# Kernel optimization log

Hardware: AMD Instinct MI355X
Metric: run time of the kernel (lower is better)

The kernel has to match this reference:

```python
import jax, jax.numpy as jnp
import numpy as np

N_NODES, N_EDGES = 100000, 800000
F_NODE, F_EDGE, N_CLASSES = 128, 16, 10


def _lin(key, fan_in, fan_out, bias=True):
    k1, k2 = jax.random.split(key)
    W = jax.random.normal(k1, (fan_in, fan_out), jnp.float32) * 0.05
    if bias:
        b = jax.random.normal(k2, (fan_out,), jnp.float32) * 0.05
        return W, b
    return (W,)


def setup_inputs() -> dict:
    key = jax.random.key(0)
    ks = jax.random.split(key, 24)
    inp = {
        "x": jax.random.normal(ks[0], (N_NODES, F_NODE), jnp.float32),
        "edge_index": jax.random.randint(ks[1], (2, N_EDGES), 0, N_NODES, jnp.int64 if jax.config.jax_enable_x64 else jnp.int32),
        "edge_attr": jax.random.normal(ks[2], (N_EDGES, F_EDGE), jnp.float32),
    }
    dims = [(F_NODE, 128), (128, 128), (128, 256)]  # (in_channels, out_channels) per layer
    i = 3
    for li, (din, dout) in enumerate(dims, start=1):
        inp[f"Wq{li}"], inp[f"bq{li}"] = _lin(ks[i], din, dout); i += 1
        inp[f"Wk{li}"], inp[f"bk{li}"] = _lin(ks[i], din, dout); i += 1
        inp[f"Wv{li}"], inp[f"bv{li}"] = _lin(ks[i], din, dout); i += 1
        (inp[f"We{li}"],) = _lin(ks[i], F_EDGE, dout, bias=False); i += 1  # PyG lin_edge: bias=False
        inp[f"Ws{li}"], inp[f"bs{li}"] = _lin(ks[i], din, dout); i += 1  # root/skip weight
    inp["Wc"], inp["bc"] = _lin(ks[i], 256, N_CLASSES)
    return inp


def transformer_conv(x, src, dst, edge_attr, Wq, bq, Wk, bk, Wv, bv, We, Ws, bs):
    """PyG TransformerConv, heads=1, concat=True, root_weight=True."""
    N = x.shape[0]
    C = Wq.shape[1]
    q = x @ Wq + bq                      # [N, C]
    k = x @ Wk + bk                      # [N, C]
    v = x @ Wv + bv                      # [N, C]
    e = edge_attr @ We                   # [E, C] edge-conditioned term
    # per-edge attention logits: <q_i, k_j + e_ij> / sqrt(C)
    alpha = jnp.sum(q[dst] * (k[src] + e), axis=-1) / jnp.sqrt(jnp.float32(C))  # [E]
    # segment softmax over edges sharing a destination node
    m = jax.ops.segment_max(alpha, dst, num_segments=N)
    p = jnp.exp(alpha - m[dst])
    s = jax.ops.segment_sum(p, dst, num_segments=N)
    a = p / (s[dst] + 1e-16)
    # scatter-aggregate weighted messages (value_j + edge term)
    out = jax.ops.segment_sum(a[:, None] * (v[src] + e), dst, num_segments=N)  # [N, C]
    return out + x @ Ws + bs             # root/skip connection


def reference(x, edge_index, edge_attr,
              Wq1, bq1, Wk1, bk1, Wv1, bv1, We1, Ws1, bs1,
              Wq2, bq2, Wk2, bk2, Wv2, bv2, We2, Ws2, bs2,
              Wq3, bq3, Wk3, bk3, Wv3, bv3, We3, Ws3, bs3,
              Wc, bc):
    src, dst = edge_index[0], edge_index[1]
    h = transformer_conv(x, src, dst, edge_attr, Wq1, bq1, Wk1, bk1, Wv1, bv1, We1, Ws1, bs1)
    h = jax.nn.relu(h)  # dropout is identity in eval mode
    h = transformer_conv(h, src, dst, edge_attr, Wq2, bq2, Wk2, bk2, Wv2, bv2, We2, Ws2, bs2)
    h = jax.nn.relu(h)
    h = transformer_conv(h, src, dst, edge_attr, Wq3, bq3, Wk3, bk3, Wv3, bv3, We3, Ws3, bs3)
    return h @ Wc + bc                   # [N, num_classes]
```

## Files before the change

### kernel.cpp

```cpp
#include <hip/hip_runtime.h>
#include <math.h>


typedef unsigned int uint;
typedef unsigned short ushort;
typedef __bf16 bf16x8 __attribute__((ext_vector_type(8)));
typedef float f32x4 __attribute__((ext_vector_type(4)));

__device__ __forceinline__ ushort f2bf(float f) {
    uint u = __float_as_uint(f);
    u += 0x7fffu + ((u >> 16) & 1u);
    return (ushort)(u >> 16);
}
__device__ __forceinline__ float bf2f(ushort h) {
    return __uint_as_float(((uint)h) << 16);
}
__device__ __forceinline__ void unpack8(uint4 t, float* o) {
    o[0] = bf2f((ushort)(t.x & 0xffffu)); o[1] = bf2f((ushort)(t.x >> 16));
    o[2] = bf2f((ushort)(t.y & 0xffffu)); o[3] = bf2f((ushort)(t.y >> 16));
    o[4] = bf2f((ushort)(t.z & 0xffffu)); o[5] = bf2f((ushort)(t.z >> 16));
    o[6] = bf2f((ushort)(t.w & 0xffffu)); o[7] = bf2f((ushort)(t.w >> 16));
}

__global__ void k_zero(uint* p, int n) {
    int i = blockIdx.x * 256 + threadIdx.x;
    if (i < n) p[i] = 0u;
}

__global__ void k_hist(const int* __restrict__ dst, uint* __restrict__ counts, int E, int N) {
    int e = blockIdx.x * 256 + threadIdx.x;
    if (e < E) {
        int d = dst[e];
        d = (d < 0) ? 0 : (d >= N ? N - 1 : d);
        atomicAdd(&counts[d], 1u);
    }
}

__global__ void k_scan1(const uint* __restrict__ counts, uint* __restrict__ bsum, int n) {
    __shared__ uint sm[256];
    int tid = threadIdx.x;
    int base = blockIdx.x * 1024 + tid * 4;
    uint s = 0;
#pragma unroll
    for (int j = 0; j < 4; ++j)
        if (base + j < n) s += counts[base + j];
    sm[tid] = s;
    __syncthreads();
    for (int d = 128; d > 0; d >>= 1) {
        if (tid < d) sm[tid] += sm[tid + d];
        __syncthreads();
    }
    if (tid == 0) bsum[blockIdx.x] = sm[0];
}

__global__ void k_scan2(uint* bsum, int nb) {
    if (threadIdx.x == 0 && blockIdx.x == 0) {
        uint run = 0;
        for (int i = 0; i < nb; ++i) { uint v = bsum[i]; bsum[i] = run; run += v; }
    }
}

__global__ void k_scan3(const uint* __restrict__ counts, const uint* __restrict__ bsum,
                        uint* __restrict__ row_ptr, int n, int E) {
    __shared__ uint sm[256];
    int tid = threadIdx.x;
    int base = blockIdx.x * 1024 + tid * 4;
    uint local[4];
    uint s = 0;
#pragma unroll
    for (int j = 0; j < 4; ++j) {
        local[j] = (base + j < n) ? counts[base + j] : 0u;
        s += local[j];
    }
    sm[tid] = s;
    __syncthreads();
    for (int d = 1; d < 256; d <<= 1) {
        uint v = (tid >= d) ? sm[tid - d] : 0u;
        __syncthreads();
        sm[tid] += v;
        __syncthreads();
    }
    uint run = sm[tid] - s + bsum[blockIdx.x];
#pragma unroll
    for (int j = 0; j < 4; ++j)
        if (base + j < n) { row_ptr[base + j] = run; run += local[j]; }
    if (blockIdx.x == 0 && tid == 0) row_ptr[n] = (uint)E;
}

__global__ void k_fill(const int* __restrict__ ei, const uint* __restrict__ row_ptr,
                       uint* __restrict__ cursor, int2* __restrict__ srcid, int E, int N) {
    int e = blockIdx.x * 256 + threadIdx.x;
    if (e >= E) return;
    int s = ei[e];
    int d = ei[E + e];
    s = (s < 0) ? 0 : (s >= N ? N - 1 : s);
    d = (d < 0) ? 0 : (d >= N ? N - 1 : d);
    uint idx = row_ptr[d] + atomicAdd(&cursor[d], 1u);
    srcid[idx] = make_int2(s, e);
}

__global__ void k_cvt(const float4* __restrict__ in, ushort4* __restrict__ outp, int n4) {
    int i = blockIdx.x * 256 + threadIdx.x;
    if (i >= n4) return;
    float4 v = in[i];
    ushort4 o;
    o.x = f2bf(v.x); o.y = f2bf(v.y); o.z = f2bf(v.z); o.w = f2bf(v.w);
    outp[i] = o;
}

__global__ void k_packg(const float* __restrict__ Wq, const float* __restrict__ bq,
                        const float* __restrict__ We, float* __restrict__ Wgf,
                        float* __restrict__ bgf, int C) {
    int id = blockIdx.x * 256 + threadIdx.x;
    if (id < 2048) {
        int k = id >> 4, f = id & 15;
        float s = 0.f;
        for (int c = 0; c < C; ++c) s = fmaf(Wq[k * C + c], We[f * C + c], s);
        Wgf[id] = s;
    } else if (id < 2064) {
        int f = id - 2048;
        float s = 0.f;
        for (int c = 0; c < C; ++c) s = fmaf(bq[c], We[f * C + c], s);
        bgf[f] = s;
    }
}

__global__ void k_packw(const float* __restrict__ Wq, const float* __restrict__ Wk,
                        const float* __restrict__ Wv, const float* __restrict__ Ws,
                        const float* __restrict__ Wgf, ushort* __restrict__ Bp, int C) {
    int nct = (4 * C + 16) >> 4;
    int total = 4 * nct * 512;
    int id = blockIdx.x * 256 + threadIdx.x;
    if (id >= total) return;
    int j = id & 7;
    int rest = id >> 3;
    int lane = rest & 63;
    rest >>= 6;
    int ct = rest % nct;
    int kt = rest / nct;
    int k = kt * 32 + ((lane >> 4) << 3) + j;
    int c = (ct << 4) + (lane & 15);
    float w;
    if (c < 4 * C) {
        int mat = c / C, cc = c % C;
        const float* W = (mat == 0) ? Wq : (mat == 1) ? Wk : (mat == 2) ? Wv : Ws;
        w = W[k * C + cc];
    } else {
        w = Wgf[k * 16 + (c - 4 * C)];
    }
    Bp[id] = f2bf(w);
}

__global__ void k_bias(const float* __restrict__ bq, const float* __restrict__ bk,
                       const float* __restrict__ bv, const float* __restrict__ bs,
                       const float* __restrict__ bgf, float* __restrict__ outp, int C) {
    int c = blockIdx.x * 256 + threadIdx.x;
    if (c >= 4 * C + 16) return;
    float v;
    if (c < 4 * C) {
        int mat = c / C, cc = c % C;
        const float* b = (mat == 0) ? bq : (mat == 1) ? bk : (mat == 2) ? bv : bs;
        v = b[cc];
    } else {
        v = bgf[c - 4 * C];
    }
    outp[c] = v;
}

__global__ __launch_bounds__(256) void k_gemm(const ushort* __restrict__ A,
                                              const ushort* __restrict__ Bp,
                                              const float* __restrict__ bias,
                                              ushort* __restrict__ H,
                                              ushort* __restrict__ S,
                                              ushort* __restrict__ g, int C) {
    int fourC = 4 * C, threeC = 3 * C;
    int P = fourC + 16;
    int nct = P >> 4;
    int lane = threadIdx.x & 63;
    int wave = threadIdx.x >> 6;
    int quad = lane >> 4;
    int r = lane & 15;
    int m0 = blockIdx.y << 4;
    int c0 = (blockIdx.x << 8) + (wave << 6);
    int ct0 = c0 >> 4;
    if (ct0 >= nct) return;
    int row = m0 + r;

    f32x4 acc[4];
#pragma unroll
    for (int i = 0; i < 4; ++i) acc[i] = (f32x4){0.f, 0.f, 0.f, 0.f};

#pragma unroll
    for (int kk = 0; kk < 4; ++kk) {
        bf16x8 a = *(const bf16x8*)(A + (size_t)row * 128 + kk * 32 + (quad << 3));
#pragma unroll
        for (int i = 0; i < 4; ++i) {
            if (ct0 + i < nct) {
                bf16x8 b = *(const bf16x8*)(Bp + ((size_t)((kk * nct + ct0 + i) << 6) + lane) * 8);
                acc[i] = __builtin_amdgcn_mfma_f32_16x16x32_bf16(a, b, acc[i], 0, 0, 0);
            }
        }
    }
#pragma unroll
    for (int i = 0; i < 4; ++i) {
        int cc = c0 + (i << 4) + r;
        if (cc >= P) continue;
        float bi = bias[cc];
#pragma unroll
        for (int reg = 0; reg < 4; ++reg) {
            int rr = m0 + (quad << 2) + reg;
            ushort val = f2bf(acc[i][reg] + bi);
            if (cc < threeC)      H[(size_t)rr * threeC + cc] = val;
            else if (cc < fourC)  S[(size_t)rr * C + (cc - threeC)] = val;
            else                  g[(size_t)rr * 16 + (cc - fourC)] = val;
        }
    }
}

template <int C, int GSIZE, bool RELU>
__global__ __launch_bounds__(256, 6) void k_edge(const ushort* __restrict__ H,
                                                 ushort* __restrict__ S,
                                                 const ushort* __restrict__ g,
                                                 const uint* __restrict__ row_ptr,
                                                 const int2* __restrict__ srcid,
                                                 const float* __restrict__ eattr,
                                                 const float* __restrict__ We,
                                                 int N) {
    constexpr int VR = C / GSIZE;
    constexpr int TH = 3 * C;
    constexpr int GPB = 256 / GSIZE;
    __shared__ float swex[GPB][17];
    const float scale = (C == 128) ? 0.08838834764831843f : 0.0625f;
    const float foldk = 16.0f / (float)GSIZE;

    int lane = threadIdx.x & (GSIZE - 1);
    int grp = threadIdx.x / GSIZE;
    int f = lane & 15;
    int node = blockIdx.x * GPB + grp;
    if (node >= N) return;

    float q[VR];
    {
        uint4 tt = *(const uint4*)(H + (size_t)node * TH + lane * VR);
        unpack8(tt, q);
    }
    float gl = bf2f(g[(size_t)node * 16 + f]);
    uint beg = row_ptr[node], end = row_ptr[node + 1];

    float l = 0.f, w = 0.f;
    float acc[VR];
#pragma unroll
    for (int j = 0; j < VR; ++j) acc[j] = 0.f;

    for (uint t = beg; t < end; t += 2) {
        bool has1 = (t + 1 < end);
        int2 se0 = srcid[t];
        int2 se1 = has1 ? srcid[t + 1] : se0;
        float at0 = eattr[(size_t)se0.y * 16 + f];
        float at1 = eattr[(size_t)se1.y * 16 + f];
        uint4 k0 = *(const uint4*)(H + (size_t)se0.x * TH + C + lane * VR);
        uint4 v0 = *(const uint4*)(H + (size_t)se0.x * TH + 2 * C + lane * VR);
        uint4 k1, v1;
        if (has1) {
            k1 = *(const uint4*)(H + (size_t)se1.x * TH + C + lane * VR);
            v1 = *(const uint4*)(H + (size_t)se1.x * TH + 2 * C + lane * VR);
        }
        float kf[VR];
        unpack8(k0, kf);
        float p0 = foldk * at0 * gl;
#pragma unroll
        for (int j = 0; j < VR; ++j) p0 = fmaf(q[j], kf[j], p0);
        float p1 = 0.f;
        if (has1) {
            unpack8(k1, kf);
            p1 = foldk * at1 * gl;
#pragma unroll
            for (int j = 0; j < VR; ++j) p1 = fmaf(q[j], kf[j], p1);
        }
        p0 += __shfl_xor(p0, 1); p1 += __shfl_xor(p1, 1);
        p0 += __shfl_xor(p0, 2); p1 += __shfl_xor(p1, 2);
        p0 += __shfl_xor(p0, 4); p1 += __shfl_xor(p1, 4);
        p0 += __shfl_xor(p0, 8); p1 += __shfl_xor(p1, 8);
        if (GSIZE == 32) { p0 += __shfl_xor(p0, 16); p1 += __shfl_xor(p1, 16); }
        float e0 = __expf(p0 * scale);
        float e1 = has1 ? __expf(p1 * scale) : 0.f;
        l += e0 + e1;
        w = fmaf(e0, at0, w);
        w = fmaf(e1, at1, w);
        float vf[VR];
        unpack8(v0, vf);
#pragma unroll
        for (int j = 0; j < VR; ++j) acc[j] = fmaf(e0, vf[j], acc[j]);
        if (has1) {
            unpack8(v1, vf);
#pragma unroll
            for (int j = 0; j < VR; ++j) acc[j] = fmaf(e1, vf[j], acc[j]);
        }
    }

    float inv = 1.f / (l + 1e-16f);
    if (lane < 16) swex[grp][lane] = w;
    float ew[VR];
#pragma unroll
    for (int j = 0; j < VR; ++j) ew[j] = 0.f;
#pragma unroll
    for (int f2 = 0; f2 < 16; ++f2) {
        float wf = swex[grp][f2];
        const float* wrow = We + f2 * C + lane * VR;
#pragma unroll
        for (int u = 0; u < VR / 4; ++u) {
            float4 cv = *(const float4*)(wrow + u * 4);
            ew[u * 4 + 0] = fmaf(wf, cv.x, ew[u * 4 + 0]);
            ew[u * 4 + 1] = fmaf(wf, cv.y, ew[u * 4 + 1]);
            ew[u * 4 + 2] = fmaf(wf, cv.z, ew[u * 4 + 2]);
            ew[u * 4 + 3] = fmaf(wf, cv.w, ew[u * 4 + 3]);
        }
    }
    ushort* srow = S + (size_t)node * C + lane * VR;
    uint4 skv = *(const uint4*)srow;
    float sk[8];
    unpack8(skv, sk);
    uint4 ov;
    uint* op = (uint*)&ov;
#pragma unroll
    for (int h = 0; h < 4; ++h) {
        float o0 = (acc[2 * h] + ew[2 * h]) * inv + sk[2 * h];
        float o1 = (acc[2 * h + 1] + ew[2 * h + 1]) * inv + sk[2 * h + 1];
        if (RELU) { o0 = fmaxf(o0, 0.f); o1 = fmaxf(o1, 0.f); }
        op[h] = (uint)f2bf(o0) | ((uint)f2bf(o1) << 16);
    }
    *(uint4*)srow = ov;
}

__global__ void k_cls(const ushort* __restrict__ h, const float* __restrict__ Wc,
                      const float* __restrict__ bc, float* __restrict__ outp, int N) {
    int t = blockIdx.x * 256 + threadIdx.x;
    int node = t >> 4;
    int c = t & 15;
    if (node >= N || c >= 10) return;
    const ushort* hr = h + (size_t)node * 256;
    float acc = 0.f;
#pragma unroll 4
    for (int k4 = 0; k4 < 64; ++k4) {
        uint2 u = *(const uint2*)(hr + k4 * 4);
        float h0 = bf2f((ushort)(u.x & 0xffffu));
        float h1 = bf2f((ushort)(u.x >> 16));
        float h2 = bf2f((ushort)(u.y & 0xffffu));
        float h3 = bf2f((ushort)(u.y >> 16));
        int kb = k4 * 4;
        acc = fmaf(h0, Wc[(kb + 0) * 10 + c], acc);
        acc = fmaf(h1, Wc[(kb + 1) * 10 + c], acc);
        acc = fmaf(h2, Wc[(kb + 2) * 10 + c], acc);
        acc = fmaf(h3, Wc[(kb + 3) * 10 + c], acc);
    }
    outp[node * 10 + c] = acc + bc[c];
}

extern "C" void kernel_launch(void* const* d_in, const int* in_sizes, int n_in,
                              void* d_out, int out_size, void* d_ws, size_t ws_size,
                              hipStream_t stream) {
    const float* x = (const float*)d_in[0];
    const int* ei = (const int*)d_in[1];
    const float* eattr = (const float*)d_in[2];
    const int N = in_sizes[0] / 128;
    const int E = in_sizes[1] / 2;

    const float* Wq[3], *bq[3], *Wk[3], *bk[3], *Wv[3], *bv[3], *We[3], *Ws[3], *bs[3];
    for (int li = 0; li < 3; ++li) {
        int base = 3 + li * 9;
        Wq[li] = (const float*)d_in[base + 0];
        bq[li] = (const float*)d_in[base + 1];
        Wk[li] = (const float*)d_in[base + 2];
        bk[li] = (const float*)d_in[base + 3];
        Wv[li] = (const float*)d_in[base + 4];
        bv[li] = (const float*)d_in[base + 5];
        We[li] = (const float*)d_in[base + 6];
        Ws[li] = (const float*)d_in[base + 7];
        bs[li] = (const float*)d_in[base + 8];
    }
    const float* Wc = (const float*)d_in[30];
    const float* bc = (const float*)d_in[31];

    size_t off = 0;
    char* base = (char*)d_ws;
    auto alloc = [&](size_t bytes) -> void* {
        void* p = base + off;
        off = (off + bytes + 255) & ~(size_t)255;
        return p;
    };
    ushort* SA = (ushort*)alloc((size_t)N * 256 * 2);
    ushort* SB = (ushort*)alloc((size_t)N * 128 * 2);
    ushort* H  = (ushort*)alloc((size_t)N * 768 * 2);
    ushort* gbuf = (ushort*)alloc((size_t)N * 16 * 2);
    ushort* Bp = (ushort*)alloc(140000 * 2);
    float* biasc = (float*)alloc(1040 * 4);
    float* Wgf = (float*)alloc(2048 * 4);
    float* bgf = (float*)alloc(16 * 4);
    uint* row_ptr = (uint*)alloc((size_t)(N + 1) * 4);
    uint* counts = (uint*)alloc((size_t)N * 4);
    uint* cursor = (uint*)alloc((size_t)N * 4);
    uint* bsum = (uint*)alloc(1024 * 4);
    int2* srcid = (int2*)alloc((size_t)E * 8);

    ushort* xb = SB;

    int nb = (N + 1023) / 1024;

    k_zero<<<(N + 255) / 256, 256, 0, stream>>>(counts, N);
    k_zero<<<(N + 255) / 256, 256, 0, stream>>>(cursor, N);
    k_hist<<<(E + 255) / 256, 256, 0, stream>>>(ei + E, counts, E, N);
    k_scan1<<<nb, 256, 0, stream>>>(counts, bsum, N);
    k_scan2<<<1, 64, 0, stream>>>(bsum, nb);
    k_scan3<<<nb, 256, 0, stream>>>(counts, bsum, row_ptr, N, E);
    k_fill<<<(E + 255) / 256, 256, 0, stream>>>(ei, row_ptr, cursor, srcid, E, N);

    int n4 = N * 128 / 4;
    k_cvt<<<(n4 + 255) / 256, 256, 0, stream>>>((const float4*)x, (ushort4*)xb, n4);

    for (int li = 0; li < 3; ++li) {
        int C = (li == 2) ? 256 : 128;
        int P = 4 * C + 16;
        int packTotal = 4 * (P >> 4) * 512;
        const ushort* A = (li == 0) ? xb : (li == 1) ? SA : SB;
        ushort* Sout = (li == 1) ? SB : SA;

        k_packg<<<9, 256, 0, stream>>>(Wq[li], bq[li], We[li], Wgf, bgf, C);
        k_packw<<<(packTotal + 255) / 256, 256, 0, stream>>>(Wq[li], Wk[li], Wv[li], Ws[li], Wgf, Bp, C);
        k_bias<<<(P + 255) / 256, 256, 0, stream>>>(bq[li], bk[li], bv[li], bs[li], bgf, biasc, C);
        k_gemm<<<dim3((P + 255) / 256, N / 16), 256, 0, stream>>>(A, Bp, biasc, H, Sout, gbuf, C);
        if (li == 2)
            k_edge<256, 32, false><<<(N * 32 + 255) / 256, 256, 0, stream>>>(H, Sout, gbuf, row_ptr, srcid, eattr, We[li], N);
        else
            k_edge<128, 16, true><<<(N * 16 + 255) / 256, 256, 0, stream>>>(H, Sout, gbuf, row_ptr, srcid, eattr, We[li], N);
    }

    k_cls<<<(N * 16 + 255) / 256, 256, 0, stream>>>(SA, Wc, bc, (float*)d_out, N);
}
```

Baseline: 1.021 ms.

## Register-tile GEMM over 64 rows and fuse small setup kernels

The projection GEMM now has each wave compute four 16-row tiles per B fragment, so every B load from the packed weights is reused across 64 rows instead of 16. Out-of-range rows are clamped on load and skipped on store. Separately, weight packing and bias packing are merged into one kernel, and the two zeroing launches become one by allocating counts and cursor contiguously, which cuts launch count. The larger register tile raises VGPR pressure (sixteen accumulators per wave) and may reduce occupancy.

```diff
diff --git a/kernel.cpp b/kernel.cpp
--- a/kernel.cpp
+++ b/kernel.cpp
@@ -125,46 +125,46 @@
     }
 }
 
-__global__ void k_packw(const float* __restrict__ Wq, const float* __restrict__ Wk,
-                        const float* __restrict__ Wv, const float* __restrict__ Ws,
-                        const float* __restrict__ Wgf, ushort* __restrict__ Bp, int C) {
-    int nct = (4 * C + 16) >> 4;
+__global__ void k_packwb(const float* __restrict__ Wq, const float* __restrict__ bq,
+                         const float* __restrict__ Wk, const float* __restrict__ bk,
+                         const float* __restrict__ Wv, const float* __restrict__ bv,
+                         const float* __restrict__ Ws, const float* __restrict__ bs,
+                         const float* __restrict__ Wgf, const float* __restrict__ bgf,
+                         ushort* __restrict__ Bp, float* __restrict__ biasc, int C) {
+    int P = 4 * C + 16;
+    int nct = P >> 4;
     int total = 4 * nct * 512;
     int id = blockIdx.x * 256 + threadIdx.x;
-    if (id >= total) return;
-    int j = id & 7;
-    int rest = id >> 3;
-    int lane = rest & 63;
-    rest >>= 6;
-    int ct = rest % nct;
-    int kt = rest / nct;
-    int k = kt * 32 + ((lane >> 4) << 3) + j;
-    int c = (ct << 4) + (lane & 15);
-    float w;
-    if (c < 4 * C) {
-        int mat = c / C, cc = c % C;
-        const float* W = (mat == 0) ? Wq : (mat == 1) ? Wk : (mat == 2) ? Wv : Ws;
-        w = W[k * C + cc];
-    } else {
-        w = Wgf[k * 16 + (c - 4 * C)];
-    }
-    Bp[id] = f2bf(w);
-}
-
-__global__ void k_bias(const float* __restrict__ bq, const float* __restrict__ bk,
-                       const float* __restrict__ bv, const float* __restrict__ bs,
-                       const float* __restrict__ bgf, float* __restrict__ outp, int C) {
-    int c = blockIdx.x * 256 + threadIdx.x;
-    if (c >= 4 * C + 16) return;
-    float v;
-    if (c < 4 * C) {
-        int mat = c / C, cc = c % C;
-        const float* b = (mat == 0) ? bq : (mat == 1) ? bk : (mat == 2) ? bv : bs;
-        v = b[cc];
-    } else {
-        v = bgf[c - 4 * C];
-    }
-    outp[c] = v;
+    if (id < total) {
+        int j = id & 7;
+        int rest = id >> 3;
+        int lane = rest & 63;
+        rest >>= 6;
+        int ct = rest % nct;
+        int kt = rest / nct;
+        int k = kt * 32 + ((lane >> 4) << 3) + j;
+        int c = (ct << 4) + (lane & 15);
+        float w;
+        if (c < 4 * C) {
+            int mat = c / C, cc = c % C;
+            const float* W = (mat == 0) ? Wq : (mat == 1) ? Wk : (mat == 2) ? Wv : Ws;
+            w = W[k * C + cc];
+        } else {
+            w = Wgf[k * 16 + (c - 4 * C)];
+        }
+        Bp[id] = f2bf(w);
+    } else if (id < total + P) {
+        int c = id - total;
+        float v;
+        if (c < 4 * C) {
+            int mat = c / C, cc = c % C;
+            const float* b = (mat == 0) ? bq : (mat == 1) ? bk : (mat == 2) ? bv : bs;
+            v = b[cc];
+        } else {
+            v = bgf[c - 4 * C];
+        }
+        biasc[c] = v;
+    }
 }
 
 __global__ __launch_bounds__(256) void k_gemm(const ushort* __restrict__ A,
@@ -172,7 +172,7 @@
                                               const float* __restrict__ bias,
                                               ushort* __restrict__ H,
                                               ushort* __restrict__ S,
-                                              ushort* __restrict__ g, int C) {
+                                              ushort* __restrict__ g, int C, int N) {
     int fourC = 4 * C, threeC = 3 * C;
     int P = fourC + 16;
     int nct = P >> 4;
@@ -180,39 +180,51 @@
     int wave = threadIdx.x >> 6;
     int quad = lane >> 4;
     int r = lane & 15;
-    int m0 = blockIdx.y << 4;
-    int c0 = (blockIdx.x << 8) + (wave << 6);
-    int ct0 = c0 >> 4;
+    int m0 = blockIdx.y << 6;
+    int ct0 = (blockIdx.x << 4) + (wave << 2);
     if (ct0 >= nct) return;
-    int row = m0 + r;
-
-    f32x4 acc[4];
-#pragma unroll
-    for (int i = 0; i < 4; ++i) acc[i] = (f32x4){0.f, 0.f, 0.f, 0.f};
+
+    f32x4 acc[4][4];
+#pragma unroll
+    for (int rt = 0; rt < 4; ++rt)
+#pragma unroll
+        for (int i = 0; i < 4; ++i) acc[rt][i] = (f32x4){0.f, 0.f, 0.f, 0.f};
 
 #pragma unroll
     for (int kk = 0; kk < 4; ++kk) {
-        bf16x8 a = *(const bf16x8*)(A + (size_t)row * 128 + kk * 32 + (quad << 3));
+        bf16x8 a[4];
+#pragma unroll
+        for (int rt = 0; rt < 4; ++rt) {
+            int row = m0 + rt * 16 + r;
+            if (row >= N) row = N - 1;
+            a[rt] = *(const bf16x8*)(A + (size_t)row * 128 + kk * 32 + (quad << 3));
+        }
 #pragma unroll
         for (int i = 0; i < 4; ++i) {
             if (ct0 + i < nct) {
                 bf16x8 b = *(const bf16x8*)(Bp + ((size_t)((kk * nct + ct0 + i) << 6) + lane) * 8);
-                acc[i] = __builtin_amdgcn_mfma_f32_16x16x32_bf16(a, b, acc[i], 0, 0, 0);
+#pragma unroll
+                for (int rt = 0; rt < 4; ++rt)
+                    acc[rt][i] = __builtin_amdgcn_mfma_f32_16x16x32_bf16(a[rt], b, acc[rt][i], 0, 0, 0);
             }
         }
     }
 #pragma unroll
     for (int i = 0; i < 4; ++i) {
-        int cc = c0 + (i << 4) + r;
+        int cc = ((ct0 + i) << 4) + r;
         if (cc >= P) continue;
         float bi = bias[cc];
 #pragma unroll
-        for (int reg = 0; reg < 4; ++reg) {
-            int rr = m0 + (quad << 2) + reg;
-            ushort val = f2bf(acc[i][reg] + bi);
-            if (cc < threeC)      H[(size_t)rr * threeC + cc] = val;
-            else if (cc < fourC)  S[(size_t)rr * C + (cc - threeC)] = val;
-            else                  g[(size_t)rr * 16 + (cc - fourC)] = val;
+        for (int rt = 0; rt < 4; ++rt) {
+#pragma unroll
+            for (int reg = 0; reg < 4; ++reg) {
+                int rr = m0 + rt * 16 + (quad << 2) + reg;
+                if (rr >= N) continue;
+                ushort val = f2bf(acc[rt][i][reg] + bi);
+                if (cc < threeC)      H[(size_t)rr * threeC + cc] = val;
+                else if (cc < fourC)  S[(size_t)rr * C + (cc - threeC)] = val;
+                else                  g[(size_t)rr * 16 + (cc - fourC)] = val;
+            }
         }
     }
 }
@@ -397,8 +409,8 @@
     float* Wgf = (float*)alloc(2048 * 4);
     float* bgf = (float*)alloc(16 * 4);
     uint* row_ptr = (uint*)alloc((size_t)(N + 1) * 4);
-    uint* counts = (uint*)alloc((size_t)N * 4);
-    uint* cursor = (uint*)alloc((size_t)N * 4);
+    uint* counts = (uint*)alloc((size_t)N * 2 * 4);
+    uint* cursor = counts + N;
     uint* bsum = (uint*)alloc(1024 * 4);
     int2* srcid = (int2*)alloc((size_t)E * 8);
 
@@ -406,8 +418,7 @@
 
     int nb = (N + 1023) / 1024;
 
-    k_zero<<<(N + 255) / 256, 256, 0, stream>>>(counts, N);
-    k_zero<<<(N + 255) / 256, 256, 0, stream>>>(cursor, N);
+    k_zero<<<(2 * N + 255) / 256, 256, 0, stream>>>(counts, 2 * N);
     k_hist<<<(E + 255) / 256, 256, 0, stream>>>(ei + E, counts, E, N);
     k_scan1<<<nb, 256, 0, stream>>>(counts, bsum, N);
     k_scan2<<<1, 64, 0, stream>>>(bsum, nb);
@@ -417,21 +428,27 @@
     int n4 = N * 128 / 4;
     k_cvt<<<(n4 + 255) / 256, 256, 0, stream>>>((const float4*)x, (ushort4*)xb, n4);
 
+    int gy = (N + 63) / 64;
+
     for (int li = 0; li < 3; ++li) {
         int C = (li == 2) ? 256 : 128;
         int P = 4 * C + 16;
-        int packTotal = 4 * (P >> 4) * 512;
+        int nct = P >> 4;
+        int packTotal = 4 * nct * 512 + P;
         const ushort* A = (li == 0) ? xb : (li == 1) ? SA : SB;
         ushort* Sout = (li == 1) ? SB : SA;
 
         k_packg<<<9, 256, 0, stream>>>(Wq[li], bq[li], We[li], Wgf, bgf, C);
-        k_packw<<<(packTotal + 255) / 256, 256, 0, stream>>>(Wq[li], Wk[li], Wv[li], Ws[li], Wgf, Bp, C);
-        k_bias<<<(P + 255) / 256, 256, 0, stream>>>(bq[li], bk[li], bv[li], bs[li], bgf, biasc, C);
-        k_gemm<<<dim3((P + 255) / 256, N / 16), 256, 0, stream>>>(A, Bp, biasc, H, Sout, gbuf, C);
+        k_packwb<<<(packTotal + 255) / 256, 256, 0, stream>>>(
+            Wq[li], bq[li], Wk[li], bk[li], Wv[li], bv[li], Ws[li], bs[li],
+            Wgf, bgf, Bp, biasc, C);
+        k_gemm<<<dim3((nct + 15) / 16, gy), 256, 0, stream>>>(A, Bp, biasc, H, Sout, gbuf, C, N);
         if (li == 2)
-            k_edge<256, 32, false><<<(N * 32 + 255) / 256, 256, 0, stream>>>(H, Sout, gbuf, row_ptr, srcid, eattr, We[li], N);
+            k_edge<256, 32, false><<<(N * 32 + 255) / 256, 256, 0, stream>>>(
+                H, Sout, gbuf, row_ptr, srcid, eattr, We[li], N);
         else
-            k_edge<128, 16, true><<<(N * 16 + 255) / 256, 256, 0, stream>>>(H, Sout, gbuf, row_ptr, srcid, eattr, We[li], N);
+            k_edge<128, 16, true><<<(N * 16 + 255) / 256, 256, 0, stream>>>(
+                H, Sout, gbuf, row_ptr, srcid, eattr, We[li], N);
     }
 
     k_cls<<<(N * 16 + 255) / 256, 256, 0, stream>>>(SA, Wc, bc, (float*)d_out, N);
```

Measured after the change: 1.132 ms. +10.9%, slower.
